# Performance work log

Hardware: AMD Instinct MI355X
Metric: run time of the kernel (lower is better)

## Reference

```python
import jax, jax.numpy as jnp
import numpy as np

DIM = 96
NH = 8
HID = int(DIM * 2.66)  # 255
B, H, W = 2, 128, 128


def _conv(x, w, groups=1, pad=0):
    # NCHW conv, stride 1
    return jax.lax.conv_general_dilated(
        x, w, (1, 1), ((pad, pad), (pad, pad)),
        feature_group_count=groups,
        dimension_numbers=('NCHW', 'OIHW', 'NCHW'))


def _ln(x, w, b):
    # WithBias LayerNorm over the channel axis (torch does to_3d -> LN(dim) -> to_4d)
    mu = x.mean(axis=1, keepdims=True)
    var = ((x - mu) ** 2).mean(axis=1, keepdims=True)
    return (x - mu) * jax.lax.rsqrt(var + 1e-5) * w[None, :, None, None] + b[None, :, None, None]


def setup_inputs() -> dict:
    key = jax.random.key(0)
    ks = jax.random.split(key, 16)
    d, h2, h4 = DIM, 2 * HID, 4 * HID
    def n(k, shape, s):
        return jax.random.normal(k, shape, jnp.float32) * s
    return {
        'x': jax.random.normal(ks[0], (B, d, H, W), jnp.float32),
        'norm1_w': jnp.ones((d,), jnp.float32), 'norm1_b': jnp.zeros((d,), jnp.float32),
        'qkv_w': n(ks[1], (3 * d, d, 1, 1), 0.05),
        'qkv_dw_w': n(ks[2], (3 * d, 1, 3, 3), 0.1),
        'proj_w': n(ks[3], (d, d, 1, 1), 0.05),
        'temperature': jnp.ones((NH, 1, 1), jnp.float32),
        'thresholdweight': 0.2 * jnp.ones((4, 1, 1, 1), jnp.float32),
        'attn_w1': n(ks[4], (4, NH, NH), 0.2), 'attn_b1': jnp.zeros((4, NH), jnp.float32),
        'attn_w2': n(ks[5], (4, NH, NH), 0.2), 'attn_b2': jnp.zeros((4, NH), jnp.float32),
        'norm2_w': jnp.ones((d,), jnp.float32), 'norm2_b': jnp.zeros((d,), jnp.float32),
        'in_w': n(ks[6], (h2, d, 1, 1), 0.05),
        'main_w': n(ks[7], (h4, 1, 3, 3), 0.1),   # groups=2*HID, 2 out per group
        'lp_w': n(ks[8], (h4, 1, 3, 3), 0.1),     # depthwise
        'hp_w': n(ks[9], (h4, 1, 3, 3), 0.1),     # depthwise
        'ld_w': n(ks[10], (HID, 4, 3, 3), 0.1),   # groups=HID, 4 in per group
        'hd_w': n(ks[11], (HID, 4, 3, 3), 0.1),
        'out_w': n(ks[12], (d, h2, 1, 1), 0.05),
    }


def reference(x, norm1_w, norm1_b, qkv_w, qkv_dw_w, proj_w, temperature,
              thresholdweight, attn_w1, attn_b1, attn_w2, attn_b2,
              norm2_w, norm2_b, in_w, main_w, lp_w, hp_w, ld_w, hd_w, out_w):
    b, c, hh, ww = x.shape
    ch = c // NH
    # ---- STS channel attention ----
    xn = _ln(x, norm1_w, norm1_b)
    qkv = _conv(_conv(xn, qkv_w), qkv_dw_w, groups=3 * c, pad=1)
    q, k, v = jnp.split(qkv, 3, axis=1)
    q = q.reshape(b, NH, ch, hh * ww)
    k = k.reshape(b, NH, ch, hh * ww)
    v = v.reshape(b, NH, ch, hh * ww)
    q = q / jnp.maximum(jnp.linalg.norm(q, axis=-1, keepdims=True), 1e-12)
    k = k / jnp.maximum(jnp.linalg.norm(k, axis=-1, keepdims=True), 1e-12)
    attn = jnp.einsum('bhcn,bhdn->bhcd', q, k) * temperature[None]  # [b,NH,ch,ch]

    def sts_gen(w1, b1, w2, b2):
        a_abs = jnp.abs(attn)
        avg = a_abs.mean(axis=(-2, -1))                       # [b, NH] (GAP)
        g = jax.nn.sigmoid(jnp.maximum(avg @ w1.T + b1, 0.0) @ w2.T + b2)
        thr = (avg * g)[:, :, None, None]
        return jnp.sign(attn) * jnp.maximum(a_abs - thr, 0.0)

    comp = jax.vmap(sts_gen)(attn_w1, attn_b1, attn_w2, attn_b2)  # [4,b,NH,ch,ch]
    comp = jax.nn.softmax(comp, axis=-1)
    attn_c = jnp.sum(comp * thresholdweight.reshape(4, 1, 1, 1, 1), axis=0)
    out = jnp.einsum('bhcd,bhdn->bhcn', attn_c, v).reshape(b, c, hh, ww)
    x = x + _conv(out, proj_w)

    # ---- DeCoupleConvv3 FFN ----
    y = _ln(x, norm2_w, norm2_b)
    y = _conv(y, in_w)                                         # [b, 2*HID, h, w]
    y = jax.nn.relu(_conv(y, main_w, groups=2 * HID, pad=1))   # [b, 4*HID, h, w]
    avg_w = jnp.full((4 * HID, 1, 3, 3), 1.0 / 9.0, y.dtype)   # fixed, non-trainable
    yp = jnp.pad(y, ((0, 0), (0, 0), (1, 1), (1, 1)), mode='edge')  # replicate pad
    l = _conv(yp, avg_w, groups=4 * HID, pad=0)
    hb = y - l
    l = jax.nn.relu(_conv(l, lp_w, groups=4 * HID, pad=1))
    hb = jax.nn.relu(_conv(hb, hp_w, groups=4 * HID, pad=1))
    l_tol, l_toh = jnp.split(l, [2 * HID], axis=1)
    h_toh, h_tol = jnp.split(hb, [2 * HID], axis=1)
    l2 = jax.nn.relu(_conv(jnp.concatenate([l_tol, h_tol], axis=1), ld_w, groups=HID, pad=1))
    h2 = jax.nn.relu(_conv(jnp.concatenate([h_toh, l_toh], axis=1), hd_w, groups=HID, pad=1))
    ffo = _conv(jnp.concatenate([l2, h2], axis=1), out_w)
    return x + ffo
```

## Files before the change

### kernel.cpp

```cpp
#include <hip/hip_runtime.h>
#include <hip/hip_bf16.h>
#include <hip/hip_fp16.h>

#define NB   2
#define NC   96
#define NW   128
#define NPIX 16384
#define NHD  8
#define CHD  12
#define HIDC 255
#define H2C  510
#define H4C  1020

typedef __hip_bfloat16 bf16;
typedef unsigned short u16;
typedef unsigned int   u32;
typedef __half2 h2t;

typedef __attribute__((ext_vector_type(8))) __bf16 bfrag;
typedef __attribute__((ext_vector_type(4))) float  ffrag;

__device__ __forceinline__ float bfu(u16 u)  { return __uint_as_float(((u32)u) << 16); }
__device__ __forceinline__ float bflo(u32 u) { return __uint_as_float(u << 16); }
__device__ __forceinline__ float bfhi(u32 u) { return __uint_as_float(u & 0xffff0000u); }
__device__ __forceinline__ u16 f2u16(float a) {
    bf16 x = __float2bfloat16(a); return *(u16*)&x;
}
__device__ __forceinline__ u32 packbf(float a, float b) {
    return (u32)f2u16(a) | ((u32)f2u16(b) << 16);
}
__device__ __forceinline__ uint4 pack8(const float o[8]) {
    uint4 r; r.x = packbf(o[0], o[1]); r.y = packbf(o[2], o[3]);
    r.z = packbf(o[4], o[5]); r.w = packbf(o[6], o[7]); return r;
}

__device__ __forceinline__ h2t H2u(u32 v) { return __builtin_bit_cast(h2t, v); }
__device__ __forceinline__ u32 U32h(h2t v) { return __builtin_bit_cast(u32, v); }
__device__ __forceinline__ h2t relu2(h2t v) {
    u32 r, u = U32h(v);
    asm("v_pk_max_f16 %0, %1, 0" : "=v"(r) : "v"(u));
    return H2u(r);
}
__device__ __forceinline__ h2t wtap(const h2t* a, int idx) {
    u32 u = U32h(a[idx >> 1]);
    u32 r = (idx & 1) ? ((u & 0xFFFF0000u) | (u >> 16)) : ((u << 16) | (u & 0xFFFFu));
    return H2u(r);
}

struct Trip { h2t L, C, R; };
__device__ __forceinline__ Trip shift3(h2t c2, bool repl, int lane) {
    u32 d = U32h(c2);
    u32 up = (u32)__shfl_up((int)d, 1);
    u32 dn = (u32)__shfl_down((int)d, 1);
    if (lane == 0)  up = repl ? (d << 16) : 0u;
    if (lane == 63) dn = repl ? (d >> 16) : 0u;
    Trip t; t.C = c2;
    t.L = H2u((up >> 16) | (d << 16));
    t.R = H2u((d >> 16) | (dn << 16));
    return t;
}
__device__ __forceinline__ h2t ldrow2(const u16* base, int row, int lane) {
    return ((unsigned)row < 128u) ? *(const h2t*)(base + row * NW + lane * 2) : H2u(0u);
}
#define CONV3(W, c, T, Pa, Pb, Pc)                                             \
    Pc = __hfma2(wtap(W, (c)*9+0), T.L, __hfma2(wtap(W, (c)*9+1), T.C,         \
         __hfma2(wtap(W, (c)*9+2), T.R, Pc)));                                 \
    Pb = __hfma2(wtap(W, (c)*9+3), T.L, __hfma2(wtap(W, (c)*9+4), T.C,         \
         __hfma2(wtap(W, (c)*9+5), T.R, Pb)));                                 \
    Pa = __hfma2(wtap(W, (c)*9+6), T.L, __hfma2(wtap(W, (c)*9+7), T.C,         \
         __hfma2(wtap(W, (c)*9+8), T.R, Pa)));

__global__ __launch_bounds__(64) void ffnstream_kernel(
    const u16* __restrict__ yi, const float* __restrict__ main_w,
    const float* __restrict__ lp_w, const float* __restrict__ hp_w,
    const float* __restrict__ ld_w, const float* __restrict__ hd_w,
    u16* __restrict__ cat) {
    const int lane = threadIdx.x;
    const int g = blockIdx.y;
    const int R0 = blockIdx.x * 32, R1 = R0 + 32;
    const int L0 = max(R0 - 2, 0), L1 = min(R1 + 1, 127);
    const int P0 = max(R0 - 1, 0), P1 = min(R1, 127);
    const u16* yib = yi + (size_t)blockIdx.z * H2C * NPIX;
    u16* catb = cat + (size_t)blockIdx.z * H2C * NPIX;
    const u16* s0p = yib + (size_t)(2 * g) * NPIX;
    const u16* s1p = yib + (size_t)(2 * g + 1) * NPIX;

    h2t wm[18], wl[18], wh[18], wd[18], we[18];
    {
        const float* pm = main_w + 36 * g;
        const float* pl = lp_w + 36 * g;
        const float* ph = hp_w + 36 * g;
        const float* pd = ld_w + 36 * g;
        const float* pe = hd_w + 36 * g;
        #pragma unroll
        for (int k = 0; k < 18; ++k) {
            wm[k] = __halves2half2(__float2half(pm[2*k]), __float2half(pm[2*k+1]));
            wl[k] = __halves2half2(__float2half(pl[2*k]), __float2half(pl[2*k+1]));
            wh[k] = __halves2half2(__float2half(ph[2*k]), __float2half(ph[2*k+1]));
            wd[k] = __halves2half2(__float2half(pd[2*k]), __float2half(pd[2*k+1]));
            we[k] = __halves2half2(__float2half(pe[2*k]), __float2half(pe[2*k+1]));
        }
    }
    const h2t z = H2u(0u);
    const __half k9h = __float2half(1.f / 9.f);
    const h2t k9 = __halves2half2(k9h, k9h);

    h2t ymP0[4], ymP1[4], ymP2[4];
    h2t ymRa[4], ymRb[4], ymRc[4];
    h2t lpP0[4], lpP1[4], lpP2[4];
    h2t hpP0[4], hpP1[4], hpP2[4];
    h2t cd0 = z, cd1 = z, cd2 = z;
    h2t ce0 = z, ce1 = z, ce2 = z;
    #pragma unroll
    for (int c = 0; c < 4; ++c) {
        ymP0[c] = ymP1[c] = ymP2[c] = z;
        ymRa[c] = ymRb[c] = ymRc[c] = z;
        lpP0[c] = lpP1[c] = lpP2[c] = z;
        hpP0[c] = hpP1[c] = hpP2[c] = z;
    }

    const int ys = max(R0 - 3, 0) - 1;
    const int ye = R1 + 3;
    h2t cur0 = ldrow2(s0p, ys, lane),     cur1 = ldrow2(s1p, ys, lane);
    h2t nx10 = ldrow2(s0p, ys + 1, lane), nx11 = ldrow2(s1p, ys + 1, lane);
    #pragma unroll 3
    for (int yy = ys; yy <= ye; ++yy) {
        h2t nx20 = ldrow2(s0p, yy + 2, lane), nx21 = ldrow2(s1p, yy + 2, lane);
        {
            Trip t0 = shift3(cur0, false, lane);
            Trip t1 = shift3(cur1, false, lane);
            CONV3(wm, 0, t0, ymP0[0], ymP1[0], ymP2[0]);
            CONV3(wm, 1, t0, ymP0[1], ymP1[1], ymP2[1]);
            CONV3(wm, 2, t1, ymP0[2], ymP1[2], ymP2[2]);
            CONV3(wm, 3, t1, ymP0[3], ymP1[3], ymP2[3]);
        }
        #pragma unroll
        for (int c = 0; c < 4; ++c) {
            h2t n = relu2(ymP0[c]);
            ymRc[c] = ymRb[c]; ymRb[c] = ymRa[c]; ymRa[c] = n;
            ymP0[c] = ymP1[c]; ymP1[c] = ymP2[c]; ymP2[c] = z;
        }
        int y_l = yy - 2;
        if (y_l >= L0 && y_l <= L1) {
            #pragma unroll
            for (int c = 0; c < 4; ++c) {
                h2t top = (y_l == 0)   ? ymRb[c] : ymRc[c];
                h2t bot = (y_l == 127) ? ymRb[c] : ymRa[c];
                h2t vs = __hadd2(__hadd2(top, ymRb[c]), bot);
                Trip tv = shift3(vs, true, lane);
                h2t l  = __hmul2(__hadd2(__hadd2(tv.L, tv.C), tv.R), k9);
                h2t hb = __hsub2(ymRb[c], l);
                Trip tl = shift3(l, false, lane);
                CONV3(wl, c, tl, lpP0[c], lpP1[c], lpP2[c]);
                Trip th = shift3(hb, false, lane);
                CONV3(wh, c, th, hpP0[c], hpP1[c], hpP2[c]);
            }
        }
        int y_p = yy - 3;
        {
            h2t lpN[4], hpN[4];
            #pragma unroll
            for (int c = 0; c < 4; ++c) {
                lpN[c] = relu2(lpP0[c]); hpN[c] = relu2(hpP0[c]);
                lpP0[c] = lpP1[c]; lpP1[c] = lpP2[c]; lpP2[c] = z;
                hpP0[c] = hpP1[c]; hpP1[c] = hpP2[c]; hpP2[c] = z;
            }
            if (y_p >= P0 && y_p <= P1) {
                #pragma unroll
                for (int c = 0; c < 4; ++c) {
                    bool low = (4 * g + c) < H2C;
                    h2t sld = low ? lpN[c] : hpN[c];
                    h2t shd = low ? hpN[c] : lpN[c];
                    Trip ts = shift3(sld, false, lane);
                    CONV3(wd, c, ts, cd0, cd1, cd2);
                    Trip tu = shift3(shd, false, lane);
                    CONV3(we, c, tu, ce0, ce1, ce2);
                }
            }
        }
        int y_c = yy - 4;
        if (y_c >= R0 && y_c < R1) {
            float a0 = fmaxf(__low2float(cd0), 0.f), a1 = fmaxf(__high2float(cd0), 0.f);
            float b0 = fmaxf(__low2float(ce0), 0.f), b1 = fmaxf(__high2float(ce0), 0.f);
            *(u32*)(catb + (size_t)g * NPIX + y_c * NW + lane * 2) = packbf(a0, a1);
            *(u32*)(catb + (size_t)(HIDC + g) * NPIX + y_c * NW + lane * 2) = packbf(b0, b1);
        }
        cd0 = cd1; cd1 = cd2; cd2 = z;
        ce0 = ce1; ce1 = ce2; ce2 = z;
        cur0 = nx10; cur1 = nx11;
        nx10 = nx20; nx11 = nx21;
    }
}

template <typename TOut, bool RES, int OFMT>
__global__ __launch_bounds__(256) void gemm1x1_kernel(
    const u16* __restrict__ Bm, const float* __restrict__ Am,
    const float* __restrict__ res, TOut* __restrict__ Cm,
    int M, int K, size_t strideB, size_t strideC) {
    __shared__ u16 Ash[64 * 40];
    __shared__ u16 Bsh[128 * 40];
    const u16* Bz = Bm + (size_t)blockIdx.z * strideB;
    int n0 = blockIdx.x * 128;
    int m0 = blockIdx.y * 64;
    int tid = threadIdx.x;
    int w = tid >> 6, l15 = tid & 15, q = (tid & 63) >> 4;
    int amm = tid >> 2, akc = (tid & 3) * 8;
    int bkk = tid >> 3, bs0 = tid & 7;

    ffrag acc[8];
    #pragma unroll
    for (int nt = 0; nt < 8; ++nt)
        #pragma unroll
        for (int e = 0; e < 4; ++e) acc[nt][e] = 0.f;

    for (int k0 = 0; k0 < K; k0 += 32) {
        {
            int gm = m0 + amm;
            float f[8];
            #pragma unroll
            for (int e = 0; e < 8; ++e) {
                int gk = k0 + akc + e;
                f[e] = (gm < M && gk < K) ? Am[(size_t)gm * K + gk] : 0.f;
            }
            u32* dst = (u32*)&Ash[amm * 40 + akc];
            #pragma unroll
            for (int e = 0; e < 4; ++e) dst[e] = packbf(f[2 * e], f[2 * e + 1]);
        }
        {
            int gk = k0 + bkk;
            bool ok = gk < K;
            const u16* src = Bz + (size_t)gk * NPIX + n0;
            #pragma unroll
            for (int pass = 0; pass < 2; ++pass) {
                int nn = (bs0 + pass * 8) * 8;
                if (ok) {
                    uint4 v = *(const uint4*)(src + nn);
                    Bsh[(nn + 0) * 40 + bkk] = (u16)(v.x & 0xffff);
                    Bsh[(nn + 1) * 40 + bkk] = (u16)(v.x >> 16);
                    Bsh[(nn + 2) * 40 + bkk] = (u16)(v.y & 0xffff);
                    Bsh[(nn + 3) * 40 + bkk] = (u16)(v.y >> 16);
                    Bsh[(nn + 4) * 40 + bkk] = (u16)(v.z & 0xffff);
                    Bsh[(nn + 5) * 40 + bkk] = (u16)(v.z >> 16);
                    Bsh[(nn + 6) * 40 + bkk] = (u16)(v.w & 0xffff);
                    Bsh[(nn + 7) * 40 + bkk] = (u16)(v.w >> 16);
                } else {
                    #pragma unroll
                    for (int e = 0; e < 8; ++e) Bsh[(nn + e) * 40 + bkk] = 0;
                }
            }
        }
        __syncthreads();
        bfrag af = *(const bfrag*)&Ash[(w * 16 + l15) * 40 + q * 8];
        #pragma unroll
        for (int nt = 0; nt < 8; ++nt) {
            bfrag bf = *(const bfrag*)&Bsh[(nt * 16 + l15) * 40 + q * 8];
            acc[nt] = __builtin_amdgcn_mfma_f32_16x16x32_bf16(af, bf, acc[nt], 0, 0, 0);
        }
        __syncthreads();
    }
    TOut* Cz = Cm + (size_t)blockIdx.z * strideC;
    const float* rz = res + (RES ? (size_t)blockIdx.z * strideC : 0);
    int mrow = m0 + w * 16 + q * 4;
    #pragma unroll
    for (int nt = 0; nt < 8; ++nt) {
        int col = n0 + nt * 16 + l15;
        #pragma unroll
        for (int r = 0; r < 4; ++r) {
            int row = mrow + r;
            if (row < M) {
                float v = acc[nt][r];
                if (RES) v += rz[(size_t)row * NPIX + col];
                if constexpr (OFMT == 0) {
                    ((float*)Cz)[(size_t)row * NPIX + col] = v;
                } else if constexpr (OFMT == 1) {
                    ((u16*)Cz)[(size_t)row * NPIX + col] = f2u16(v);
                } else {
                    __half hh = __float2half(v);
                    ((u16*)Cz)[(size_t)row * NPIX + col] = __builtin_bit_cast(u16, hh);
                }
            }
        }
    }
}

__global__ __launch_bounds__(256) void ln_kernel(
    const float* __restrict__ x, const float* __restrict__ g,
    const float* __restrict__ bta, u16* __restrict__ out) {
    int blk = blockIdx.x;
    int b = blk >> 9;
    int p = ((blk & 511) << 5) + (threadIdx.x & 31);
    int cg = threadIdx.x >> 5;
    const float* xb = x + (size_t)b * NC * NPIX + p;
    float v[12]; float s = 0.f, s2 = 0.f;
    #pragma unroll
    for (int j = 0; j < 12; ++j) {
        float t = xb[(size_t)(cg * 12 + j) * NPIX];
        v[j] = t; s += t; s2 += t * t;
    }
    __shared__ float ss[8][32], qq[8][32], smu[32], sinv[32];
    ss[cg][threadIdx.x & 31] = s; qq[cg][threadIdx.x & 31] = s2;
    __syncthreads();
    if (threadIdx.x < 32) {
        float S = 0.f, Q = 0.f;
        #pragma unroll
        for (int k = 0; k < 8; ++k) { S += ss[k][threadIdx.x]; Q += qq[k][threadIdx.x]; }
        float mu = S * (1.f / NC);
        float var = Q * (1.f / NC) - mu * mu;
        smu[threadIdx.x] = mu; sinv[threadIdx.x] = rsqrtf(var + 1e-5f);
    }
    __syncthreads();
    float mu = smu[threadIdx.x & 31], inv = sinv[threadIdx.x & 31];
    u16* ob = out + (size_t)b * NC * NPIX + p;
    #pragma unroll
    for (int j = 0; j < 12; ++j) {
        int c = cg * 12 + j;
        ob[(size_t)c * NPIX] = f2u16((v[j] - mu) * inv * g[c] + bta[c]);
    }
}

__device__ __forceinline__ void load_row_zpad(const u16* ib, int iy, int x0, float a[10]) {
    if (iy < 0 || iy >= NW) {
        #pragma unroll
        for (int k = 0; k < 10; ++k) a[k] = 0.f;
        return;
    }
    const u16* rp = ib + iy * NW;
    uint4 v = *(const uint4*)(rp + x0);
    a[1]=bflo(v.x); a[2]=bfhi(v.x); a[3]=bflo(v.y); a[4]=bfhi(v.y);
    a[5]=bflo(v.z); a[6]=bfhi(v.z); a[7]=bflo(v.w); a[8]=bfhi(v.w);
    a[0] = (x0 > 0)   ? bfu(rp[x0 - 1]) : 0.f;
    a[9] = (x0 < 120) ? bfu(rp[x0 + 8]) : 0.f;
}

template <bool RELU>
__global__ __launch_bounds__(256) void dwconv3x3_kernel(
    const u16* __restrict__ in, const float* __restrict__ w,
    u16* __restrict__ out, int CHN, int ICN, int idiv) {
    int id = blockIdx.x * 256 + threadIdx.x;
    int ty = id >> 4, tx = id & 15;
    int y0 = ty * 4, x0 = tx * 8;
    int b = blockIdx.y / CHN, oc = blockIdx.y % CHN;
    int ic = oc / idiv;
    const u16* ib = in + ((size_t)b * ICN + ic) * NPIX;
    float a[6][10];
    #pragma unroll
    for (int k = 0; k < 6; ++k) load_row_zpad(ib, y0 - 1 + k, x0, a[k]);
    const float* wr = w + (size_t)oc * 9;
    float w9[9];
    #pragma unroll
    for (int k = 0; k < 9; ++k) w9[k] = wr[k];
    u16* ob = out + ((size_t)b * CHN + oc) * NPIX + y0 * NW + x0;
    #pragma unroll
    for (int jr = 0; jr < 4; ++jr) {
        float o[8];
        #pragma unroll
        for (int j = 0; j < 8; ++j) {
            float s = 0.f;
            #pragma unroll
            for (int r = 0; r < 3; ++r)
                #pragma unroll
                for (int kx = 0; kx < 3; ++kx)
                    s += w9[r * 3 + kx] * a[jr + r][j + kx];
            o[j] = RELU ? fmaxf(s, 0.f) : s;
        }
        *(uint4*)(ob + jr * NW) = pack8(o);
    }
}

__global__ __launch_bounds__(256) void qknorm_kernel(
    const u16* __restrict__ qkv2, float* __restrict__ scales) {
    int r = blockIdx.x;
    int b = r / 192, ch = r % 192;
    const u16* src = qkv2 + ((size_t)b * 288 + ch) * NPIX;
    float s = 0.f;
    for (int p = threadIdx.x * 8; p < NPIX; p += 2048) {
        uint4 v = *(const uint4*)(src + p);
        float f[8];
        f[0]=bflo(v.x); f[1]=bfhi(v.x); f[2]=bflo(v.y); f[3]=bfhi(v.y);
        f[4]=bflo(v.z); f[5]=bfhi(v.z); f[6]=bflo(v.w); f[7]=bfhi(v.w);
        #pragma unroll
        for (int k = 0; k < 8; ++k) s += f[k] * f[k];
    }
    #pragma unroll
    for (int off = 32; off > 0; off >>= 1) s += __shfl_down(s, off, 64);
    __shared__ float part[4];
    int wid = threadIdx.x >> 6;
    if ((threadIdx.x & 63) == 0) part[wid] = s;
    __syncthreads();
    if (threadIdx.x == 0) {
        float tot = part[0] + part[1] + part[2] + part[3];
        scales[r] = 1.f / fmaxf(sqrtf(tot), 1e-12f);
    }
}

__global__ __launch_bounds__(256) void attn_kernel(
    const u16* __restrict__ qkv2, float* __restrict__ attn_raw) {
    int blk = blockIdx.y;
    int slice = blockIdx.x;
    int i = blk % CHD; int h = (blk / CHD) % NHD; int b = blk / (CHD * NHD);
    const u16* q = qkv2 + ((size_t)b * 288 + h * CHD + i) * NPIX;
    const u16* k = qkv2 + ((size_t)b * 288 + 96 + h * CHD) * NPIX;
    float acc[CHD];
    #pragma unroll
    for (int j = 0; j < CHD; ++j) acc[j] = 0.f;
    int p0 = slice * 4096;
    #pragma unroll
    for (int it = 0; it < 2; ++it) {
        int p = p0 + it * 2048 + threadIdx.x * 8;
        uint4 qv = *(const uint4*)(q + p);
        float qf[8];
        qf[0]=bflo(qv.x); qf[1]=bfhi(qv.x); qf[2]=bflo(qv.y); qf[3]=bfhi(qv.y);
        qf[4]=bflo(qv.z); qf[5]=bfhi(qv.z); qf[6]=bflo(qv.w); qf[7]=bfhi(qv.w);
        #pragma unroll
        for (int j = 0; j < CHD; ++j) {
            uint4 kv = *(const uint4*)(k + (size_t)j * NPIX + p);
            float s = qf[0]*bflo(kv.x) + qf[1]*bfhi(kv.x) + qf[2]*bflo(kv.y) + qf[3]*bfhi(kv.y)
                    + qf[4]*bflo(kv.z) + qf[5]*bfhi(kv.z) + qf[6]*bflo(kv.w) + qf[7]*bfhi(kv.w);
            acc[j] += s;
        }
    }
    __shared__ float part[4][CHD];
    int wid = threadIdx.x >> 6, lane = threadIdx.x & 63;
    #pragma unroll
    for (int j = 0; j < CHD; ++j) {
        float v = acc[j];
        #pragma unroll
        for (int off = 32; off > 0; off >>= 1) v += __shfl_down(v, off, 64);
        if (lane == 0) part[wid][j] = v;
    }
    __syncthreads();
    if (threadIdx.x < CHD) {
        int j = threadIdx.x;
        float d = part[0][j] + part[1][j] + part[2][j] + part[3][j];
        atomicAdd(&attn_raw[(size_t)blk * CHD + j], d);
    }
}

__global__ __launch_bounds__(256) void sts_kernel(
    const float* __restrict__ attn, const float* __restrict__ scl,
    const float* __restrict__ temp, const float* __restrict__ tw,
    const float* __restrict__ w1, const float* __restrict__ b1,
    const float* __restrict__ w2, const float* __restrict__ b2,
    float* __restrict__ attn_c) {
    int b = blockIdx.x;
    __shared__ float sat[NHD * CHD * CHD];
    __shared__ float avg[NHD];
    __shared__ float thr[4][NHD];
    for (int idx = threadIdx.x; idx < NHD * CHD * CHD; idx += 256) {
        int h = idx / (CHD * CHD); int r = idx % (CHD * CHD);
        int i = r / CHD, j = r % CHD;
        sat[idx] = attn[(size_t)b * NHD * CHD * CHD + idx]
                 * scl[b * 192 + h * CHD + i] * scl[b * 192 + 96 + h * CHD + j] * temp[h];
    }
    __syncthreads();
    if (threadIdx.x < NHD) {
        float s = 0.f;
        for (int t = 0; t < CHD * CHD; ++t) s += fabsf(sat[threadIdx.x * CHD * CHD + t]);
        avg[threadIdx.x] = s * (1.f / (CHD * CHD));
    }
    __syncthreads();
    if (threadIdx.x < 4) {
        int s = threadIdx.x;
        float t1[NHD];
        for (int hp = 0; hp < NHD; ++hp) {
            float u = b1[s * NHD + hp];
            for (int h = 0; h < NHD; ++h) u += avg[h] * w1[s * 64 + hp * NHD + h];
            t1[hp] = fmaxf(u, 0.f);
        }
        for (int hp = 0; hp < NHD; ++hp) {
            float u = b2[s * NHD + hp];
            for (int h = 0; h < NHD; ++h) u += t1[h] * w2[s * 64 + hp * NHD + h];
            float gg = 1.f / (1.f + expf(-u));
            thr[s][hp] = avg[hp] * gg;
        }
    }
    __syncthreads();
    if (threadIdx.x < NHD * CHD) {
        int h = threadIdx.x / CHD, i = threadIdx.x % CHD;
        const float* arow = sat + (h * CHD + i) * CHD;
        float acc[CHD];
        #pragma unroll
        for (int j = 0; j < CHD; ++j) acc[j] = 0.f;
        for (int s = 0; s < 4; ++s) {
            float comp[CHD]; float m = -1e30f;
            #pragma unroll
            for (int j = 0; j < CHD; ++j) {
                float a = arow[j];
                float sg = (a > 0.f) ? 1.f : ((a < 0.f) ? -1.f : 0.f);
                float c = sg * fmaxf(fabsf(a) - thr[s][h], 0.f);
                comp[j] = c; m = fmaxf(m, c);
            }
            float sum = 0.f;
            #pragma unroll
            for (int j = 0; j < CHD; ++j) { comp[j] = expf(comp[j] - m); sum += comp[j]; }
            float wts2v = tw[s] / sum;
            #pragma unroll
            for (int j = 0; j < CHD; ++j) acc[j] += wts2v * comp[j];
        }
        for (int j = 0; j < CHD; ++j)
            attn_c[(size_t)b * NHD * CHD * CHD + (h * CHD + i) * CHD + j] = acc[j];
    }
}

__global__ __launch_bounds__(256) void av_kernel(
    const float* __restrict__ attn_c, const u16* __restrict__ qkv2,
    u16* __restrict__ outv) {
    int p0 = (blockIdx.x * 256 + threadIdx.x) * 4;
    int bc = blockIdx.y;
    int b = bc / NC, hc = bc % NC; int h = hc / CHD, i = hc % CHD;
    const float* a = attn_c + ((size_t)(b * NHD + h) * CHD + i) * CHD;
    const u16* v = qkv2 + ((size_t)b * 288 + 192 + h * CHD) * NPIX;
    float av[CHD];
    #pragma unroll
    for (int j = 0; j < CHD; ++j) av[j] = a[j];
    float o[4] = {0.f, 0.f, 0.f, 0.f};
    #pragma unroll
    for (int j = 0; j < CHD; ++j) {
        uint2 t = *(const uint2*)(v + (size_t)j * NPIX + p0);
        o[0] += av[j] * bflo(t.x); o[1] += av[j] * bfhi(t.x);
        o[2] += av[j] * bflo(t.y); o[3] += av[j] * bfhi(t.y);
    }
    uint2 t; t.x = packbf(o[0], o[1]); t.y = packbf(o[2], o[3]);
    *(uint2*)(outv + ((size_t)b * NC + hc) * NPIX + p0) = t;
}

extern "C" void kernel_launch(void* const* d_in, const int* in_sizes, int n_in,
                              void* d_out, int out_size, void* d_ws, size_t ws_size,
                              hipStream_t stream) {
    const float* x       = (const float*)d_in[0];
    const float* norm1_w = (const float*)d_in[1];
    const float* norm1_b = (const float*)d_in[2];
    const float* qkv_w   = (const float*)d_in[3];
    const float* qkv_dw  = (const float*)d_in[4];
    const float* proj_w  = (const float*)d_in[5];
    const float* temp    = (const float*)d_in[6];
    const float* thw     = (const float*)d_in[7];
    const float* aw1     = (const float*)d_in[8];
    const float* ab1     = (const float*)d_in[9];
    const float* aw2     = (const float*)d_in[10];
    const float* ab2     = (const float*)d_in[11];
    const float* norm2_w = (const float*)d_in[12];
    const float* norm2_b = (const float*)d_in[13];
    const float* in_w    = (const float*)d_in[14];
    const float* main_w  = (const float*)d_in[15];
    const float* lp_w    = (const float*)d_in[16];
    const float* hp_w    = (const float*)d_in[17];
    const float* ld_w    = (const float*)d_in[18];
    const float* hd_w    = (const float*)d_in[19];
    const float* out_w   = (const float*)d_in[20];
    float* out = (float*)d_out;

    char* ws = (char*)d_ws;
    float* x1    = (float*)(ws + 0);
    u16*   xnb   = (u16*)(ws + 12582912);
    u16*   qkv1  = (u16*)(ws + 18874368);
    u16*   qkv2  = (u16*)(ws + 37748736);
    float* scl   = (float*)(ws + 56623104);
    float* attn  = (float*)(ws + 56639488);
    float* attnc = (float*)(ws + 56655872);
    char*  F0    = ws + 56672256;
    const size_t S_full = 33423360;
    bool full = ws_size >= (size_t)56672256 + S_full;

    dim3 blk(256);
    ln_kernel<<<dim3(NB * NPIX / 32), blk, 0, stream>>>(x, norm1_w, norm1_b, xnb);
    gemm1x1_kernel<u16, false, 1><<<dim3(128, 5, NB), blk, 0, stream>>>(
        xnb, qkv_w, nullptr, qkv1, 288, 96, (size_t)NC * NPIX, (size_t)288 * NPIX);
    dwconv3x3_kernel<false><<<dim3(2, NB * 288), blk, 0, stream>>>(
        qkv1, qkv_dw, qkv2, 288, 288, 1);
    qknorm_kernel<<<dim3(NB * 192), blk, 0, stream>>>(qkv2, scl);
    (void)hipMemsetAsync(attn, 0, (size_t)NB * NHD * CHD * CHD * sizeof(float), stream);
    attn_kernel<<<dim3(4, NB * NHD * CHD), blk, 0, stream>>>(qkv2, attn);
    sts_kernel<<<dim3(NB), blk, 0, stream>>>(attn, scl, temp, thw, aw1, ab1, aw2, ab2, attnc);
    av_kernel<<<dim3(16, NB * NC), blk, 0, stream>>>(attnc, qkv2, xnb);
    gemm1x1_kernel<float, true, 0><<<dim3(128, 2, NB), blk, 0, stream>>>(
        xnb, proj_w, x, x1, 96, 96, (size_t)NC * NPIX, (size_t)NC * NPIX);
    ln_kernel<<<dim3(NB * NPIX / 32), blk, 0, stream>>>(x1, norm2_w, norm2_b, xnb);
    if (full) {
        u16* yi  = qkv1;
        u16* cat = (u16*)F0;
        gemm1x1_kernel<u16, false, 2><<<dim3(128, 8, NB), blk, 0, stream>>>(
            xnb, in_w, nullptr, yi, H2C, 96, (size_t)NC * NPIX, (size_t)H2C * NPIX);
        ffnstream_kernel<<<dim3(4, HIDC, NB), dim3(64), 0, stream>>>(
            yi, main_w, lp_w, hp_w, ld_w, hd_w, cat);
        gemm1x1_kernel<float, true, 0><<<dim3(128, 2, NB), blk, 0, stream>>>(
            cat, out_w, x1, out, 96, H2C, (size_t)H2C * NPIX, (size_t)NC * NPIX);
    } else {
        for (int b = 0; b < NB; ++b) {
            u16* yi  = qkv1;
            u16* cat = qkv2;
            gemm1x1_kernel<u16, false, 2><<<dim3(128, 8, 1), blk, 0, stream>>>(
                xnb + (size_t)b * NC * NPIX, in_w, nullptr, yi, H2C, 96, 0, 0);
            ffnstream_kernel<<<dim3(4, HIDC, 1), dim3(64), 0, stream>>>(
                yi, main_w, lp_w, hp_w, ld_w, hd_w, cat);
            gemm1x1_kernel<float, true, 0><<<dim3(128, 2, 1), blk, 0, stream>>>(
                cat, out_w, x1 + (size_t)b * NC * NPIX, out + (size_t)b * NC * NPIX,
                96, H2C, 0, 0);
        }
    }
}
```

Before: 359.3 us.

## Fold attention-value mix into projection weights and halve ffnstream row tiles

Replaces the per-pixel attention-times-V kernel with a tiny kernel that premultiplies proj_w by the block-diagonal attention matrix per batch. The projection GEMM then reads V directly from qkv2 with a per-batch weight matrix, which removes one full activation write and read pass. The FFN streaming kernel also uses 16-row tiles instead of 32, doubling its grid for more parallelism at the cost of more halo recomputation. Folding the weights changes where bf16 rounding happens, since the intermediate result is no longer quantized.

```diff
diff --git a/kernel.cpp b/kernel.cpp
--- a/kernel.cpp
+++ b/kernel.cpp
@@ -77,7 +77,7 @@
     u16* __restrict__ cat) {
     const int lane = threadIdx.x;
     const int g = blockIdx.y;
-    const int R0 = blockIdx.x * 32, R1 = R0 + 32;
+    const int R0 = blockIdx.x * 16, R1 = R0 + 16;
     const int L0 = max(R0 - 2, 0), L1 = min(R1 + 1, 127);
     const int P0 = max(R0 - 1, 0), P1 = min(R1, 127);
     const u16* yib = yi + (size_t)blockIdx.z * H2C * NPIX;
@@ -196,10 +196,11 @@
 __global__ __launch_bounds__(256) void gemm1x1_kernel(
     const u16* __restrict__ Bm, const float* __restrict__ Am,
     const float* __restrict__ res, TOut* __restrict__ Cm,
-    int M, int K, size_t strideB, size_t strideC) {
+    int M, int K, size_t strideB, size_t strideC, size_t strideA) {
     __shared__ u16 Ash[64 * 40];
     __shared__ u16 Bsh[128 * 40];
     const u16* Bz = Bm + (size_t)blockIdx.z * strideB;
+    const float* Az = Am + (size_t)blockIdx.z * strideA;
     int n0 = blockIdx.x * 128;
     int m0 = blockIdx.y * 64;
     int tid = threadIdx.x;
@@ -220,7 +221,7 @@
             #pragma unroll
             for (int e = 0; e < 8; ++e) {
                 int gk = k0 + akc + e;
-                f[e] = (gm < M && gk < K) ? Am[(size_t)gm * K + gk] : 0.f;
+                f[e] = (gm < M && gk < K) ? Az[(size_t)gm * K + gk] : 0.f;
             }
             u32* dst = (u32*)&Ash[amm * 40 + akc];
             #pragma unroll
@@ -502,26 +503,22 @@
     }
 }
 
-__global__ __launch_bounds__(256) void av_kernel(
-    const float* __restrict__ attn_c, const u16* __restrict__ qkv2,
-    u16* __restrict__ outv) {
-    int p0 = (blockIdx.x * 256 + threadIdx.x) * 4;
-    int bc = blockIdx.y;
-    int b = bc / NC, hc = bc % NC; int h = hc / CHD, i = hc % CHD;
-    const float* a = attn_c + ((size_t)(b * NHD + h) * CHD + i) * CHD;
-    const u16* v = qkv2 + ((size_t)b * 288 + 192 + h * CHD) * NPIX;
-    float av[CHD];
-    #pragma unroll
-    for (int j = 0; j < CHD; ++j) av[j] = a[j];
-    float o[4] = {0.f, 0.f, 0.f, 0.f};
-    #pragma unroll
-    for (int j = 0; j < CHD; ++j) {
-        uint2 t = *(const uint2*)(v + (size_t)j * NPIX + p0);
-        o[0] += av[j] * bflo(t.x); o[1] += av[j] * bfhi(t.x);
-        o[2] += av[j] * bflo(t.y); o[3] += av[j] * bfhi(t.y);
-    }
-    uint2 t; t.x = packbf(o[0], o[1]); t.y = packbf(o[2], o[3]);
-    *(uint2*)(outv + ((size_t)b * NC + hc) * NPIX + p0) = t;
+__global__ __launch_bounds__(256) void wmix_kernel(
+    const float* __restrict__ proj_w, const float* __restrict__ attn_c,
+    float* __restrict__ Wm) {
+    int b = blockIdx.x;
+    const float* ac = attn_c + (size_t)b * NHD * CHD * CHD;
+    float* Wb = Wm + (size_t)b * NC * NC;
+    for (int idx = threadIdx.x; idx < NC * NC; idx += 256) {
+        int m = idx / NC, col = idx % NC;
+        int h = col / CHD, j = col % CHD;
+        const float* pr = proj_w + m * NC + h * CHD;
+        const float* ar = ac + (size_t)h * CHD * CHD + j;
+        float s = 0.f;
+        #pragma unroll
+        for (int i = 0; i < CHD; ++i) s += pr[i] * ar[(size_t)i * CHD];
+        Wb[idx] = s;
+    }
 }
 
 extern "C" void kernel_launch(void* const* d_in, const int* in_sizes, int n_in,
@@ -559,43 +556,45 @@
     float* attn  = (float*)(ws + 56639488);
     float* attnc = (float*)(ws + 56655872);
     char*  F0    = ws + 56672256;
+    float* Wm    = (float*)(ws + 12582912);
     const size_t S_full = 33423360;
     bool full = ws_size >= (size_t)56672256 + S_full;
 
     dim3 blk(256);
     ln_kernel<<<dim3(NB * NPIX / 32), blk, 0, stream>>>(x, norm1_w, norm1_b, xnb);
     gemm1x1_kernel<u16, false, 1><<<dim3(128, 5, NB), blk, 0, stream>>>(
-        xnb, qkv_w, nullptr, qkv1, 288, 96, (size_t)NC * NPIX, (size_t)288 * NPIX);
+        xnb, qkv_w, nullptr, qkv1, 288, 96, (size_t)NC * NPIX, (size_t)288 * NPIX, 0);
     dwconv3x3_kernel<false><<<dim3(2, NB * 288), blk, 0, stream>>>(
         qkv1, qkv_dw, qkv2, 288, 288, 1);
     qknorm_kernel<<<dim3(NB * 192), blk, 0, stream>>>(qkv2, scl);
     (void)hipMemsetAsync(attn, 0, (size_t)NB * NHD * CHD * CHD * sizeof(float), stream);
     attn_kernel<<<dim3(4, NB * NHD * CHD), blk, 0, stream>>>(qkv2, attn);
     sts_kernel<<<dim3(NB), blk, 0, stream>>>(attn, scl, temp, thw, aw1, ab1, aw2, ab2, attnc);
-    av_kernel<<<dim3(16, NB * NC), blk, 0, stream>>>(attnc, qkv2, xnb);
+    wmix_kernel<<<dim3(NB), blk, 0, stream>>>(proj_w, attnc, Wm);
     gemm1x1_kernel<float, true, 0><<<dim3(128, 2, NB), blk, 0, stream>>>(
-        xnb, proj_w, x, x1, 96, 96, (size_t)NC * NPIX, (size_t)NC * NPIX);
+        qkv2 + (size_t)192 * NPIX, Wm, x, x1, 96, 96,
+        (size_t)288 * NPIX, (size_t)NC * NPIX, (size_t)NC * NC);
     ln_kernel<<<dim3(NB * NPIX / 32), blk, 0, stream>>>(x1, norm2_w, norm2_b, xnb);
     if (full) {
         u16* yi  = qkv1;
         u16* cat = (u16*)F0;
         gemm1x1_kernel<u16, false, 2><<<dim3(128, 8, NB), blk, 0, stream>>>(
-            xnb, in_w, nullptr, yi, H2C, 96, (size_t)NC * NPIX, (size_t)H2C * NPIX);
-        ffnstream_kernel<<<dim3(4, HIDC, NB), dim3(64), 0, stream>>>(
+            xnb, in_w, nullptr, yi, H2C, 96, (size_t)NC * NPIX, (size_t)H2C * NPIX, 0);
+        ffnstream_kernel<<<dim3(8, HIDC, NB), dim3(64), 0, stream>>>(
             yi, main_w, lp_w, hp_w, ld_w, hd_w, cat);
         gemm1x1_kernel<float, true, 0><<<dim3(128, 2, NB), blk, 0, stream>>>(
-            cat, out_w, x1, out, 96, H2C, (size_t)H2C * NPIX, (size_t)NC * NPIX);
+            cat, out_w, x1, out, 96, H2C, (size_t)H2C * NPIX, (size_t)NC * NPIX, 0);
     } else {
         for (int b = 0; b < NB; ++b) {
             u16* yi  = qkv1;
             u16* cat = qkv2;
             gemm1x1_kernel<u16, false, 2><<<dim3(128, 8, 1), blk, 0, stream>>>(
-                xnb + (size_t)b * NC * NPIX, in_w, nullptr, yi, H2C, 96, 0, 0);
-            ffnstream_kernel<<<dim3(4, HIDC, 1), dim3(64), 0, stream>>>(
+                xnb + (size_t)b * NC * NPIX, in_w, nullptr, yi, H2C, 96, 0, 0, 0);
+            ffnstream_kernel<<<dim3(8, HIDC, 1), dim3(64), 0, stream>>>(
                 yi, main_w, lp_w, hp_w, ld_w, hd_w, cat);
             gemm1x1_kernel<float, true, 0><<<dim3(128, 2, 1), blk, 0, stream>>>(
                 cat, out_w, x1 + (size_t)b * NC * NPIX, out + (size_t)b * NC * NPIX,
-                96, H2C, 0, 0);
-        }
-    }
-}
+                96, H2C, 0, 0, 0);
+        }
+    }
+}
```

New measurement: 382.9 us. +6.6%, slower.
